# Kernel optimization log

Hardware: AMD Instinct MI355X
Metric: run time of the kernel (lower is better)

## Reference

```python
import jax, jax.numpy as jnp
import numpy as np

NUM_LEVELS = 16
LOG2_T = 19
TABLE_SIZE = 1 << LOG2_T
F_PER_LEVEL = 2
MIN_RES, MAX_RES = 16, 4096
N = 524288

_growth = np.exp((np.log(MAX_RES) - np.log(MIN_RES)) / (NUM_LEVELS - 1))
SCALINGS = np.floor(MIN_RES * _growth ** np.arange(NUM_LEVELS)).astype(np.float32)  # [L]
HASH_OFFSET = (np.arange(NUM_LEVELS) * TABLE_SIZE).astype(np.uint32)  # [L]
# corner selection: True -> use ceil coord, order matches torch hashed_0..hashed_7
CORNER_MASK = np.array([[1,1,1],[1,0,1],[0,0,1],[0,1,1],[1,1,0],[1,0,0],[0,0,0],[0,1,0]], dtype=bool)
PRIMES = np.array([1, 2654435761, 805459861], dtype=np.uint32)


def _hash(coords):
    # coords: uint32 [..., 3]; instant-ngp spatial hash, table size is a power of 2
    c = coords * jnp.asarray(PRIMES)
    h = c[..., 0] ^ c[..., 1] ^ c[..., 2]
    h = h & jnp.uint32(TABLE_SIZE - 1)
    return (h + jnp.asarray(HASH_OFFSET)).astype(jnp.int32)  # [..., L]


def hash_encode(pts, table):
    # pts: [N, 3] in [0,1]; table: [L*T, F]
    scaled = pts[:, None, :] * jnp.asarray(SCALINGS)[:, None]            # [N, L, 3]
    sc = jnp.ceil(scaled).astype(jnp.int32).astype(jnp.uint32)
    sf_f = jnp.floor(scaled)
    sf = sf_f.astype(jnp.int32).astype(jnp.uint32)
    offset = scaled - sf_f                                               # [N, L, 3]
    mask = jnp.asarray(CORNER_MASK)[:, None, None, :]                    # [8,1,1,3]
    coords = jnp.where(mask, sc[None], sf[None])                         # [8, N, L, 3]
    f = table[_hash(coords)]                                             # [8, N, L, F]
    wx = offset[..., 0:1]; wy = offset[..., 1:2]; wz = offset[..., 2:3]
    f_03 = f[0] * wx + f[3] * (1 - wx)
    f_12 = f[1] * wx + f[2] * (1 - wx)
    f_56 = f[5] * wx + f[6] * (1 - wx)
    f_47 = f[4] * wx + f[7] * (1 - wx)
    f0312 = f_03 * wy + f_12 * (1 - wy)
    f4756 = f_47 * wy + f_56 * (1 - wy)
    enc = f0312 * wz + f4756 * (1 - wz)                                  # [N, L, F]
    return enc.reshape(enc.shape[0], NUM_LEVELS * F_PER_LEVEL)


def setup_inputs() -> dict:
    key = jax.random.key(0)
    k1, k2, k3, k4 = jax.random.split(key, 4)
    x = jax.random.uniform(k1, (N, 6), dtype=jnp.float32)
    hash_table = (jax.random.uniform(k2, (TABLE_SIZE * NUM_LEVELS, F_PER_LEVEL), dtype=jnp.float32) * 2 - 1) * 1e-3
    w1 = jax.random.normal(k3, (64, 64), dtype=jnp.float32) * 0.05
    w2 = jax.random.normal(k4, (64, 16), dtype=jnp.float32) * 0.05
    return {"x": x, "hash_table": hash_table, "w1": w1, "w2": w2}


def reference(x, hash_table, w1, w2):
    p0, p1 = x[:, :3], x[:, 3:]                          # segment start / end
    enc = jnp.concatenate([hash_encode(p0, hash_table), hash_encode(p1, hash_table)], axis=-1)  # [N,64]
    h = jax.nn.relu(enc @ w1)                            # FullyFusedMLP: 1 hidden layer, ReLU, no bias
    out = h @ w2                                         # [N, 1+geo_feat_dim]
    density = jnp.exp(out[:, :1] - 1.0)                  # trunc_exp(x - 1)
    return jnp.concatenate([density, out[:, 1:]], axis=-1)
```

## Files before the change

kernel.cpp:

```cpp
#include <hip/hip_runtime.h>
#include <math.h>

#define NLVL 16
#define TSIZE (1u << 19)
#define PRIME_Y 2654435761u
#define PRIME_Z 805459861u
#define QSCALE 126000.0f
#define W1SCALE 254.0f

#if __has_builtin(__builtin_amdgcn_sdot4)
#define HAS_SDOT4 1
#else
#define HAS_SDOT4 0
#endif
#if __has_builtin(__builtin_amdgcn_fdot2)
#define HAS_FDOT2 1
#else
#define HAS_FDOT2 0
#endif

typedef _Float16 half2_t __attribute__((ext_vector_type(2)));

struct ScalingsArg { float s[NLVL]; };

__device__ __forceinline__ unsigned f2bf(float f) {
    unsigned u = __float_as_uint(f);
    return (u + 0x7fffu + ((u >> 16) & 1u)) >> 16;
}
__device__ __forceinline__ float bf2f(unsigned hw) { return __uint_as_float(hw << 16); }

__device__ __forceinline__ int q8(float v) {
    return __float2int_rn(fmaxf(fminf(v * QSCALE, 127.f), -127.f));
}
__device__ __forceinline__ unsigned qw8(float v) {
    return (unsigned)(__float2int_rn(fmaxf(fminf(v * W1SCALE, 127.f), -127.f))) & 0xffu;
}

__device__ __forceinline__ int dot4i8(unsigned a, unsigned b, int c) {
#if HAS_SDOT4
    return __builtin_amdgcn_sdot4((int)a, (int)b, c, false);
#else
    c += (int)(signed char)(a & 0xffu)         * (int)(signed char)(b & 0xffu);
    c += (int)(signed char)((a >> 8) & 0xffu)  * (int)(signed char)((b >> 8) & 0xffu);
    c += (int)(signed char)((a >> 16) & 0xffu) * (int)(signed char)((b >> 16) & 0xffu);
    c += (int)(signed char)(a >> 24)           * (int)(signed char)(b >> 24);
    return c;
#endif
}

__device__ __forceinline__ unsigned pkh2(float a, float b) {
    union { half2_t h; unsigned u; } cv;
    cv.h.x = (_Float16)a; cv.h.y = (_Float16)b;
    return cv.u;
}
__device__ __forceinline__ float dot2h(unsigned a, unsigned b, float c) {
    union { unsigned u; half2_t h; } ca, cb;
    ca.u = a; cb.u = b;
#if HAS_FDOT2
    return __builtin_amdgcn_fdot2(ca.h, cb.h, c, false);
#else
    return c + (float)ca.h.x * (float)cb.h.x + (float)ca.h.y * (float)cb.h.y;
#endif
}

__global__ __launch_bounds__(256) void ngp_conv(
    const float4* __restrict__ t, uint2* __restrict__ o, int n2)
{
    const int i = blockIdx.x * 256 + threadIdx.x;
    if (i < n2) {
        const float4 v = t[i];
        o[i] = make_uint2(f2bf(v.x) | (f2bf(v.y) << 16),
                          f2bf(v.z) | (f2bf(v.w) << 16));
    }
}

template<int BF>
__global__ __launch_bounds__(256) void ngp_encode_lvl(
    const float* __restrict__ x,
    const float2* __restrict__ tf,
    const unsigned* __restrict__ tb,
    unsigned* __restrict__ encq,
    ScalingsArg sca, int npts)
{
    const int pt = blockIdx.x * 256 + threadIdx.x;
    if (pt >= npts) return;
    const int l = blockIdx.y;
    const float s = sca.s[l];
    const unsigned base = (unsigned)l * TSIZE;
    const unsigned m = TSIZE - 1u;

    const float* xp = x + (size_t)pt * 6;
    const float2 v0 = *reinterpret_cast<const float2*>(xp);
    const float2 v1 = *reinterpret_cast<const float2*>(xp + 2);
    const float2 v2 = *reinterpret_cast<const float2*>(xp + 4);
    const float q[2][3] = { { v0.x, v0.y, v1.x }, { v1.y, v2.x, v2.y } };

    int qb[4];
    #pragma unroll
    for (int e = 0; e < 2; ++e) {
        const float sx = q[e][0] * s, sy = q[e][1] * s, sz = q[e][2] * s;
        const float fx = floorf(sx), fy = floorf(sy), fz = floorf(sz);
        const float wx = sx - fx, wy = sy - fy, wz = sz - fz;
        const unsigned ixf = (unsigned)(int)fx, iyf = (unsigned)(int)fy, izf = (unsigned)(int)fz;
        const unsigned ixc = (unsigned)(int)ceilf(sx);
        const unsigned iyc = (unsigned)(int)ceilf(sy);
        const unsigned izc = (unsigned)(int)ceilf(sz);
        const unsigned hyf = iyf * PRIME_Y, hyc = iyc * PRIME_Y;
        const unsigned hzf = izf * PRIME_Z, hzc = izc * PRIME_Z;
        const unsigned h0 = hyc ^ hzc, h1 = hyf ^ hzc, h2 = hyf ^ hzf, h3 = hyc ^ hzf;
        const unsigned dx = ixf ^ ixc;
        const unsigned A[4] = { (ixf ^ h0) & m, (ixf ^ h1) & m,
                                (ixf ^ h2) & m, (ixf ^ h3) & m };

        float2 cf[4], cc[4];

        if (BF) {
            unsigned uf[4], uc[4];
            if (dx == 1u) {
                #pragma unroll
                for (int j = 0; j < 4; ++j) {
                    const uint2 v = *reinterpret_cast<const uint2*>(&tb[base + (A[j] & ~1u)]);
                    const bool hi = (A[j] & 1u) != 0u;
                    uf[j] = hi ? v.y : v.x;
                    uc[j] = hi ? v.x : v.y;
                }
            } else if (dx == 3u) {
                #pragma unroll
                for (int j = 0; j < 4; ++j) {
                    const uint4 v = *reinterpret_cast<const uint4*>(&tb[base + (A[j] & ~3u)]);
                    const unsigned o = A[j] & 3u;
                    uf[j] = (o == 0u) ? v.x : (o == 1u) ? v.y : (o == 2u) ? v.z : v.w;
                    uc[j] = (o == 0u) ? v.w : (o == 1u) ? v.z : (o == 2u) ? v.y : v.x;
                }
            } else {
                #pragma unroll
                for (int j = 0; j < 4; ++j) {
                    uf[j] = tb[base + A[j]];
                    uc[j] = tb[base + ((A[j] ^ dx) & m)];
                }
            }
            #pragma unroll
            for (int j = 0; j < 4; ++j) {
                cf[j] = make_float2(bf2f(uf[j] & 0xffffu), bf2f(uf[j] >> 16));
                cc[j] = make_float2(bf2f(uc[j] & 0xffffu), bf2f(uc[j] >> 16));
            }
        } else {
            if (dx == 1u) {
                #pragma unroll
                for (int j = 0; j < 4; ++j) {
                    const float4 v = *reinterpret_cast<const float4*>(&tf[base + (A[j] & ~1u)]);
                    const bool hi = (A[j] & 1u) != 0u;
                    cf[j] = hi ? make_float2(v.z, v.w) : make_float2(v.x, v.y);
                    cc[j] = hi ? make_float2(v.x, v.y) : make_float2(v.z, v.w);
                }
            } else {
                #pragma unroll
                for (int j = 0; j < 4; ++j) {
                    cf[j] = tf[base + A[j]];
                    cc[j] = tf[base + ((A[j] ^ dx) & m)];
                }
            }
        }

        const float cx = 1.f - wx, cy = 1.f - wy, cz = 1.f - wz;
        const float g03x = cc[0].x * wx + cf[0].x * cx, g03y = cc[0].y * wx + cf[0].y * cx;
        const float g12x = cc[1].x * wx + cf[1].x * cx, g12y = cc[1].y * wx + cf[1].y * cx;
        const float g56x = cc[2].x * wx + cf[2].x * cx, g56y = cc[2].y * wx + cf[2].y * cx;
        const float g47x = cc[3].x * wx + cf[3].x * cx, g47y = cc[3].y * wx + cf[3].y * cx;
        const float t0x = g03x * wy + g12x * cy, t0y = g03y * wy + g12y * cy;
        const float t1x = g47x * wy + g56x * cy, t1y = g47y * wy + g56y * cy;
        qb[e * 2 + 0] = q8(t0x * wz + t1x * cz);
        qb[e * 2 + 1] = q8(t0y * wz + t1y * cz);
    }

    encq[(size_t)l * npts + pt] =
        (qb[0] & 0xff) | ((qb[1] & 0xff) << 8) | ((qb[2] & 0xff) << 16) | ((qb[3] & 0xff) << 24);
}

__global__ __launch_bounds__(256) void ngp_mlp2i(
    const unsigned* __restrict__ encq,
    const float* __restrict__ w1,
    const float* __restrict__ w2,
    float* __restrict__ out, int npts)
{
    __shared__ unsigned lw1i[64 * 16];
    __shared__ unsigned lw2h[16 * 32];
    const int tid = threadIdx.x;

    #pragma unroll
    for (int t = 0; t < 4; ++t) {
        const int idx = tid * 4 + t;
        const int j = idx >> 4, g = idx & 15;
        const unsigned b0 = qw8(w1[(2 * g) * 64 + j]);
        const unsigned b1 = qw8(w1[(2 * g + 1) * 64 + j]);
        const unsigned b2 = qw8(w1[(32 + 2 * g) * 64 + j]);
        const unsigned b3 = qw8(w1[(33 + 2 * g) * 64 + j]);
        lw1i[j * 16 + g] = b0 | (b1 << 8) | (b2 << 16) | (b3 << 24);
    }
    #pragma unroll
    for (int t = 0; t < 2; ++t) {
        const int idx = tid * 2 + t;
        const int c = idx >> 5, jp = idx & 31;
        lw2h[c * 32 + jp] = pkh2(w2[(2 * jp) * 16 + c], w2[(2 * jp + 1) * 16 + c]);
    }
    __syncthreads();

    const int base = (blockIdx.x * 256 + tid) * 2;
    if (base >= npts) return;

    unsigned ev0[16], ev1[16];
    #pragma unroll
    for (int l = 0; l < NLVL; ++l) {
        const uint2 v = *reinterpret_cast<const uint2*>(&encq[(size_t)l * npts + base]);
        ev0[l] = v.x; ev1[l] = v.y;
    }

    const float s1 = 1.0f / (QSCALE * W1SCALE);
    unsigned hp0[32], hp1[32];
    #pragma unroll
    for (int jp = 0; jp < 32; ++jp) {
        const int j0 = 2 * jp, j1 = 2 * jp + 1;
        int a00 = 0, a10 = 0, a01 = 0, a11 = 0;
        #pragma unroll
        for (int g4 = 0; g4 < 4; ++g4) {
            const uint4 w = *reinterpret_cast<const uint4*>(&lw1i[j0 * 16 + g4 * 4]);
            a00 = dot4i8(ev0[g4 * 4 + 0], w.x, a00); a10 = dot4i8(ev1[g4 * 4 + 0], w.x, a10);
            a00 = dot4i8(ev0[g4 * 4 + 1], w.y, a00); a10 = dot4i8(ev1[g4 * 4 + 1], w.y, a10);
            a00 = dot4i8(ev0[g4 * 4 + 2], w.z, a00); a10 = dot4i8(ev1[g4 * 4 + 2], w.z, a10);
            a00 = dot4i8(ev0[g4 * 4 + 3], w.w, a00); a10 = dot4i8(ev1[g4 * 4 + 3], w.w, a10);
        }
        #pragma unroll
        for (int g4 = 0; g4 < 4; ++g4) {
            const uint4 w = *reinterpret_cast<const uint4*>(&lw1i[j1 * 16 + g4 * 4]);
            a01 = dot4i8(ev0[g4 * 4 + 0], w.x, a01); a11 = dot4i8(ev1[g4 * 4 + 0], w.x, a11);
            a01 = dot4i8(ev0[g4 * 4 + 1], w.y, a01); a11 = dot4i8(ev1[g4 * 4 + 1], w.y, a11);
            a01 = dot4i8(ev0[g4 * 4 + 2], w.z, a01); a11 = dot4i8(ev1[g4 * 4 + 2], w.z, a11);
            a01 = dot4i8(ev0[g4 * 4 + 3], w.w, a01); a11 = dot4i8(ev1[g4 * 4 + 3], w.w, a11);
        }
        hp0[jp] = pkh2(fmaxf((float)a00, 0.f) * s1, fmaxf((float)a01, 0.f) * s1);
        hp1[jp] = pkh2(fmaxf((float)a10, 0.f) * s1, fmaxf((float)a11, 0.f) * s1);
    }

    float* op0 = out + (size_t)base * 16;
    const bool p1 = (base + 1 < npts);
    for (int c = 0; c < 16; ++c) {
        float s0 = 0.f, s1v = 0.f;
        #pragma unroll
        for (int jq = 0; jq < 8; ++jq) {
            const uint4 w = *reinterpret_cast<const uint4*>(&lw2h[c * 32 + jq * 4]);
            s0  = dot2h(hp0[jq * 4 + 0], w.x, s0);  s1v = dot2h(hp1[jq * 4 + 0], w.x, s1v);
            s0  = dot2h(hp0[jq * 4 + 1], w.y, s0);  s1v = dot2h(hp1[jq * 4 + 1], w.y, s1v);
            s0  = dot2h(hp0[jq * 4 + 2], w.z, s0);  s1v = dot2h(hp1[jq * 4 + 2], w.z, s1v);
            s0  = dot2h(hp0[jq * 4 + 3], w.w, s0);  s1v = dot2h(hp1[jq * 4 + 3], w.w, s1v);
        }
        if (c == 0) { s0 = expf(s0 - 1.0f); s1v = expf(s1v - 1.0f); }
        op0[c] = s0;
        if (p1) op0[16 + c] = s1v;
    }
}

__global__ __launch_bounds__(256) void ngp_fused(
    const float* __restrict__ x,
    const float2* __restrict__ table,
    const float* __restrict__ w1,
    const float* __restrict__ w2,
    float* __restrict__ out,
    ScalingsArg sca, int npts)
{
    __shared__ float lw1[64 * 64];
    __shared__ float lw2[64 * 16];
    const int tid = threadIdx.x;
    #pragma unroll
    for (int i = 0; i < 16; ++i) lw1[tid + 256 * i] = w1[tid + 256 * i];
    #pragma unroll
    for (int i = 0; i < 4; ++i)  lw2[tid + 256 * i] = w2[tid + 256 * i];
    __syncthreads();

    const int gid = blockIdx.x * 256 + tid;
    if (gid >= npts) return;

    const float* xp = x + (size_t)gid * 6;
    float2 v0 = *reinterpret_cast<const float2*>(xp);
    float2 v1 = *reinterpret_cast<const float2*>(xp + 2);
    float2 v2 = *reinterpret_cast<const float2*>(xp + 4);
    float Pt[6] = { v0.x, v0.y, v1.x, v1.y, v2.x, v2.y };

    float enc[64];
    #pragma unroll
    for (int p = 0; p < 2; ++p) {
        const float qx = Pt[p * 3 + 0], qy = Pt[p * 3 + 1], qz = Pt[p * 3 + 2];
        #pragma unroll
        for (int l = 0; l < NLVL; ++l) {
            const float s = sca.s[l];
            const float sx = qx * s, sy = qy * s, sz = qz * s;
            const float fx = floorf(sx), fy = floorf(sy), fz = floorf(sz);
            const float wx = sx - fx, wy = sy - fy, wz = sz - fz;
            const unsigned ixf = (unsigned)(int)fx, iyf = (unsigned)(int)fy, izf = (unsigned)(int)fz;
            const unsigned ixc = (unsigned)(int)ceilf(sx);
            const unsigned iyc = (unsigned)(int)ceilf(sy);
            const unsigned izc = (unsigned)(int)ceilf(sz);
            const unsigned hyf = iyf * PRIME_Y, hyc = iyc * PRIME_Y;
            const unsigned hzf = izf * PRIME_Z, hzc = izc * PRIME_Z;
            const unsigned mm = TSIZE - 1u;
            const unsigned bs = (unsigned)l * TSIZE;
            const float2 f0 = table[((ixc ^ hyc ^ hzc) & mm) + bs];
            const float2 f1 = table[((ixc ^ hyf ^ hzc) & mm) + bs];
            const float2 f2 = table[((ixf ^ hyf ^ hzc) & mm) + bs];
            const float2 f3 = table[((ixf ^ hyc ^ hzc) & mm) + bs];
            const float2 f4 = table[((ixc ^ hyc ^ hzf) & mm) + bs];
            const float2 f5 = table[((ixc ^ hyf ^ hzf) & mm) + bs];
            const float2 f6 = table[((ixf ^ hyf ^ hzf) & mm) + bs];
            const float2 f7 = table[((ixf ^ hyc ^ hzf) & mm) + bs];
            const float cx = 1.f - wx, cy = 1.f - wy, cz = 1.f - wz;
            const float g03x = f0.x * wx + f3.x * cx, g03y = f0.y * wx + f3.y * cx;
            const float g12x = f1.x * wx + f2.x * cx, g12y = f1.y * wx + f2.y * cx;
            const float g56x = f5.x * wx + f6.x * cx, g56y = f5.y * wx + f6.y * cx;
            const float g47x = f4.x * wx + f7.x * cx, g47y = f4.y * wx + f7.y * cx;
            const float t0x = g03x * wy + g12x * cy, t0y = g03y * wy + g12y * cy;
            const float t1x = g47x * wy + g56x * cy, t1y = g47y * wy + g56y * cy;
            enc[p * 32 + l * 2 + 0] = t0x * wz + t1x * cz;
            enc[p * 32 + l * 2 + 1] = t0y * wz + t1y * cz;
        }
    }

    float o[16];
    #pragma unroll
    for (int i = 0; i < 16; ++i) o[i] = 0.f;
    for (int jb = 0; jb < 64; jb += 8) {
        float acc[8];
        #pragma unroll
        for (int jj = 0; jj < 8; ++jj) acc[jj] = 0.f;
        #pragma unroll
        for (int k = 0; k < 64; ++k) {
            const float e = enc[k];
            const float4* wrow = reinterpret_cast<const float4*>(&lw1[k * 64 + jb]);
            const float4 wa = wrow[0], wb = wrow[1];
            acc[0] += e * wa.x; acc[1] += e * wa.y; acc[2] += e * wa.z; acc[3] += e * wa.w;
            acc[4] += e * wb.x; acc[5] += e * wb.y; acc[6] += e * wb.z; acc[7] += e * wb.w;
        }
        #pragma unroll
        for (int jj = 0; jj < 8; ++jj) {
            const float hv = fmaxf(acc[jj], 0.f);
            const float4* w2row = reinterpret_cast<const float4*>(&lw2[(jb + jj) * 16]);
            const float4 wa = w2row[0], wb = w2row[1], wc = w2row[2], wd = w2row[3];
            o[0]  += hv * wa.x; o[1]  += hv * wa.y; o[2]  += hv * wa.z; o[3]  += hv * wa.w;
            o[4]  += hv * wb.x; o[5]  += hv * wb.y; o[6]  += hv * wb.z; o[7]  += hv * wb.w;
            o[8]  += hv * wc.x; o[9]  += hv * wc.y; o[10] += hv * wc.z; o[11] += hv * wc.w;
            o[12] += hv * wd.x; o[13] += hv * wd.y; o[14] += hv * wd.z; o[15] += hv * wd.w;
        }
    }
    o[0] = expf(o[0] - 1.0f);
    float4* op = reinterpret_cast<float4*>(out + (size_t)gid * 16);
    op[0] = make_float4(o[0],  o[1],  o[2],  o[3]);
    op[1] = make_float4(o[4],  o[5],  o[6],  o[7]);
    op[2] = make_float4(o[8],  o[9],  o[10], o[11]);
    op[3] = make_float4(o[12], o[13], o[14], o[15]);
}

extern "C" void kernel_launch(void* const* d_in, const int* in_sizes, int n_in,
                              void* d_out, int out_size, void* d_ws, size_t ws_size,
                              hipStream_t stream) {
    const float*  x     = (const float*)d_in[0];
    const float2* table = (const float2*)d_in[1];
    const float*  w1    = (const float*)d_in[2];
    const float*  w2    = (const float*)d_in[3];
    float* out = (float*)d_out;
    const int npts = in_sizes[0] / 6;

    ScalingsArg sca;
    const double growth = exp((log(4096.0) - log(16.0)) / 15.0);
    for (int i = 0; i < NLVL; ++i)
        sca.s[i] = (float)floor(16.0 * pow(growth, (double)i));

    const size_t tbl_bytes = (size_t)NLVL * TSIZE * 4u;
    const size_t enc_bytes = (size_t)NLVL * (size_t)npts * 4u;
    const int bpl = (npts + 255) / 256;
    const dim3 gEnc(bpl, NLVL);
    const int mlp_blocks = ((npts + 1) / 2 + 255) / 256;

    if (ws_size >= tbl_bytes + enc_bytes) {
        unsigned* tb  = (unsigned*)d_ws;
        unsigned* enc = (unsigned*)((char*)d_ws + tbl_bytes);
        const int n2 = (NLVL * TSIZE) / 2;
        ngp_conv<<<(n2 + 255) / 256, 256, 0, stream>>>((const float4*)table, (uint2*)tb, n2);
        ngp_encode_lvl<1><<<gEnc, 256, 0, stream>>>(x, nullptr, tb, enc, sca, npts);
        ngp_mlp2i<<<mlp_blocks, 256, 0, stream>>>(enc, w1, w2, out, npts);
    } else if (ws_size >= enc_bytes) {
        unsigned* enc = (unsigned*)d_ws;
        ngp_encode_lvl<0><<<gEnc, 256, 0, stream>>>(x, table, nullptr, enc, sca, npts);
        ngp_mlp2i<<<mlp_blocks, 256, 0, stream>>>(enc, w1, w2, out, npts);
    } else {
        ngp_fused<<<(npts + 255) / 256, 256, 0, stream>>>(x, table, w1, w2, out, sca, npts);
    }
}
```

Measured before the change: 390.5 us.

## Use dense corner-quad grids for coarse levels and block-aligned loads for fine levels

For the four coarsest levels, a new kernel precomputes dense per-cell quads of the four xy-corner bf16 entries, so each encode point fetches two 16-byte records instead of eight scattered hashed entries. Only the remaining twelve levels are converted to bf16. Fine levels now always load one aligned uint4 block that serves both x-corners when they fall in the same block, with a fallback load otherwise. The cost is an extra precompute kernel, a larger workspace, and a level-dependent branch inside the encode kernel.

```diff
diff --git a/kernel.cpp b/kernel.cpp
--- a/kernel.cpp
+++ b/kernel.cpp
@@ -22,12 +22,14 @@
 typedef _Float16 half2_t __attribute__((ext_vector_type(2)));
 
 struct ScalingsArg { float s[NLVL]; };
+struct QuadArg { int off[4]; int res[4]; };
 
 __device__ __forceinline__ unsigned f2bf(float f) {
     unsigned u = __float_as_uint(f);
     return (u + 0x7fffu + ((u >> 16) & 1u)) >> 16;
 }
 __device__ __forceinline__ float bf2f(unsigned hw) { return __uint_as_float(hw << 16); }
+__device__ __forceinline__ unsigned pkbf2(float2 v) { return f2bf(v.x) | (f2bf(v.y) << 16); }
 
 __device__ __forceinline__ int q8(float v) {
     return __float2int_rn(fmaxf(fminf(v * QSCALE, 127.f), -127.f));
@@ -63,15 +65,138 @@
 #endif
 }
 
-__global__ __launch_bounds__(256) void ngp_conv(
-    const float4* __restrict__ t, uint2* __restrict__ o, int n2)
+__device__ __forceinline__ unsigned pick4(uint4 q, int sel) {
+    const unsigned a = (sel & 1) ? q.y : q.x;
+    const unsigned b = (sel & 1) ? q.w : q.z;
+    return (sel & 2) ? b : a;
+}
+
+__global__ __launch_bounds__(256) void ngp_conv12(
+    const float4* __restrict__ src, uint2* __restrict__ o, int n2)
 {
     const int i = blockIdx.x * 256 + threadIdx.x;
     if (i < n2) {
-        const float4 v = t[i];
+        const float4 v = src[i];
         o[i] = make_uint2(f2bf(v.x) | (f2bf(v.y) << 16),
                           f2bf(v.z) | (f2bf(v.w) << 16));
     }
+}
+
+__global__ __launch_bounds__(256) void ngp_quad(
+    const float2* __restrict__ tf, uint4* __restrict__ quads, QuadArg qa)
+{
+    const int l = blockIdx.y;
+    const int res = qa.res[l];
+    const int n = (res + 1) * res * res;
+    const int idx = blockIdx.x * 256 + threadIdx.x;
+    if (idx >= n) return;
+    const int xq = idx % res;
+    const int t1 = idx / res;
+    const int yq = t1 % res;
+    const int zq = t1 / res;
+    const unsigned m = TSIZE - 1u;
+    const unsigned base = (unsigned)l * TSIZE;
+    const unsigned hy0 = (unsigned)yq * PRIME_Y, hy1 = (unsigned)(yq + 1) * PRIME_Y;
+    const unsigned hz  = (unsigned)zq * PRIME_Z;
+    const unsigned x0 = (unsigned)xq, x1 = (unsigned)(xq + 1);
+    const float2 e00 = tf[((x0 ^ hy0 ^ hz) & m) + base];
+    const float2 e10 = tf[((x1 ^ hy0 ^ hz) & m) + base];
+    const float2 e01 = tf[((x0 ^ hy1 ^ hz) & m) + base];
+    const float2 e11 = tf[((x1 ^ hy1 ^ hz) & m) + base];
+    quads[qa.off[l] + idx] = make_uint4(pkbf2(e00), pkbf2(e10), pkbf2(e01), pkbf2(e11));
+}
+
+__global__ __launch_bounds__(256) void ngp_encode2(
+    const float* __restrict__ x,
+    const unsigned* __restrict__ tbHi,
+    const uint4* __restrict__ quads,
+    unsigned* __restrict__ encq,
+    ScalingsArg sca, QuadArg qa, int npts)
+{
+    const int pt = blockIdx.x * 256 + threadIdx.x;
+    if (pt >= npts) return;
+    const int l = blockIdx.y;
+    const float s = sca.s[l];
+    const unsigned m = TSIZE - 1u;
+
+    const float* xp = x + (size_t)pt * 6;
+    const float2 v0 = *reinterpret_cast<const float2*>(xp);
+    const float2 v1 = *reinterpret_cast<const float2*>(xp + 2);
+    const float2 v2 = *reinterpret_cast<const float2*>(xp + 4);
+    const float q[2][3] = { { v0.x, v0.y, v1.x }, { v1.y, v2.x, v2.y } };
+
+    int qb[4];
+    #pragma unroll
+    for (int e = 0; e < 2; ++e) {
+        const float sx = q[e][0] * s, sy = q[e][1] * s, sz = q[e][2] * s;
+        const float fx = floorf(sx), fy = floorf(sy), fz = floorf(sz);
+        const float wx = sx - fx, wy = sy - fy, wz = sz - fz;
+        const unsigned ixf = (unsigned)(int)fx, iyf = (unsigned)(int)fy, izf = (unsigned)(int)fz;
+        const unsigned ixc = (unsigned)(int)ceilf(sx);
+        const unsigned iyc = (unsigned)(int)ceilf(sy);
+        const unsigned izc = (unsigned)(int)ceilf(sz);
+
+        float2 cc[4], cf[4];
+
+        if (l < 4) {
+            const int res = qa.res[l];
+            const int dxs = (int)(ixc - ixf);
+            const int dys = (int)(iyc - iyf);
+            const uint4* Q = quads + qa.off[l];
+            const int rowf = (int)iyf * res + (int)ixf;
+            const uint4 qzc = Q[(int)izc * (res * res) + rowf];
+            const uint4 qzf = Q[(int)izf * (res * res) + rowf];
+            const int selcc = dys * 2 + dxs;
+            const int selfc = dys * 2;
+            const int selcf = dxs;
+            const unsigned u0 = pick4(qzc, selcc);
+            const unsigned u1 = pick4(qzc, selcf);
+            const unsigned u2 = qzc.x;
+            const unsigned u3 = pick4(qzc, selfc);
+            const unsigned u4 = pick4(qzf, selcc);
+            const unsigned u5 = pick4(qzf, selcf);
+            const unsigned u6 = qzf.x;
+            const unsigned u7 = pick4(qzf, selfc);
+            cc[0] = make_float2(bf2f(u0 & 0xffffu), bf2f(u0 >> 16));
+            cf[0] = make_float2(bf2f(u3 & 0xffffu), bf2f(u3 >> 16));
+            cc[1] = make_float2(bf2f(u1 & 0xffffu), bf2f(u1 >> 16));
+            cf[1] = make_float2(bf2f(u2 & 0xffffu), bf2f(u2 >> 16));
+            cc[2] = make_float2(bf2f(u5 & 0xffffu), bf2f(u5 >> 16));
+            cf[2] = make_float2(bf2f(u6 & 0xffffu), bf2f(u6 >> 16));
+            cc[3] = make_float2(bf2f(u4 & 0xffffu), bf2f(u4 >> 16));
+            cf[3] = make_float2(bf2f(u7 & 0xffffu), bf2f(u7 >> 16));
+        } else {
+            const unsigned base = (unsigned)(l - 4) * TSIZE;
+            const unsigned hyf = iyf * PRIME_Y, hyc = iyc * PRIME_Y;
+            const unsigned hzf = izf * PRIME_Z, hzc = izc * PRIME_Z;
+            const unsigned H[4] = { hyc ^ hzc, hyf ^ hzc, hyf ^ hzf, hyc ^ hzf };
+            const unsigned dx = ixf ^ ixc;
+            #pragma unroll
+            for (int j = 0; j < 4; ++j) {
+                const unsigned A  = (ixf ^ H[j]) & m;
+                const unsigned Ax = A ^ dx;
+                const uint4 blk = *reinterpret_cast<const uint4*>(&tbHi[base + (A & ~3u)]);
+                const unsigned uf = pick4(blk, (int)(A & 3u));
+                unsigned uc = pick4(blk, (int)(Ax & 3u));
+                if (dx > 3u) uc = tbHi[base + Ax];
+                cf[j] = make_float2(bf2f(uf & 0xffffu), bf2f(uf >> 16));
+                cc[j] = make_float2(bf2f(uc & 0xffffu), bf2f(uc >> 16));
+            }
+        }
+
+        const float cx = 1.f - wx, cy = 1.f - wy, cz = 1.f - wz;
+        const float g03x = cc[0].x * wx + cf[0].x * cx, g03y = cc[0].y * wx + cf[0].y * cx;
+        const float g12x = cc[1].x * wx + cf[1].x * cx, g12y = cc[1].y * wx + cf[1].y * cx;
+        const float g56x = cc[2].x * wx + cf[2].x * cx, g56y = cc[2].y * wx + cf[2].y * cx;
+        const float g47x = cc[3].x * wx + cf[3].x * cx, g47y = cc[3].y * wx + cf[3].y * cx;
+        const float t0x = g03x * wy + g12x * cy, t0y = g03y * wy + g12y * cy;
+        const float t1x = g47x * wy + g56x * cy, t1y = g47y * wy + g56y * cy;
+        qb[e * 2 + 0] = q8(t0x * wz + t1x * cz);
+        qb[e * 2 + 1] = q8(t0y * wz + t1y * cz);
+    }
+
+    encq[(size_t)l * npts + pt] =
+        (qb[0] & 0xff) | ((qb[1] & 0xff) << 8) | ((qb[2] & 0xff) << 16) | ((qb[3] & 0xff) << 24);
 }
 
 template<int BF>
@@ -111,57 +236,22 @@
         const unsigned dx = ixf ^ ixc;
         const unsigned A[4] = { (ixf ^ h0) & m, (ixf ^ h1) & m,
                                 (ixf ^ h2) & m, (ixf ^ h3) & m };
-
         float2 cf[4], cc[4];
-
-        if (BF) {
-            unsigned uf[4], uc[4];
-            if (dx == 1u) {
-                #pragma unroll
-                for (int j = 0; j < 4; ++j) {
-                    const uint2 v = *reinterpret_cast<const uint2*>(&tb[base + (A[j] & ~1u)]);
-                    const bool hi = (A[j] & 1u) != 0u;
-                    uf[j] = hi ? v.y : v.x;
-                    uc[j] = hi ? v.x : v.y;
-                }
-            } else if (dx == 3u) {
-                #pragma unroll
-                for (int j = 0; j < 4; ++j) {
-                    const uint4 v = *reinterpret_cast<const uint4*>(&tb[base + (A[j] & ~3u)]);
-                    const unsigned o = A[j] & 3u;
-                    uf[j] = (o == 0u) ? v.x : (o == 1u) ? v.y : (o == 2u) ? v.z : v.w;
-                    uc[j] = (o == 0u) ? v.w : (o == 1u) ? v.z : (o == 2u) ? v.y : v.x;
-                }
-            } else {
-                #pragma unroll
-                for (int j = 0; j < 4; ++j) {
-                    uf[j] = tb[base + A[j]];
-                    uc[j] = tb[base + ((A[j] ^ dx) & m)];
-                }
-            }
+        if (dx == 1u) {
             #pragma unroll
             for (int j = 0; j < 4; ++j) {
-                cf[j] = make_float2(bf2f(uf[j] & 0xffffu), bf2f(uf[j] >> 16));
-                cc[j] = make_float2(bf2f(uc[j] & 0xffffu), bf2f(uc[j] >> 16));
+                const float4 v = *reinterpret_cast<const float4*>(&tf[base + (A[j] & ~1u)]);
+                const bool hi = (A[j] & 1u) != 0u;
+                cf[j] = hi ? make_float2(v.z, v.w) : make_float2(v.x, v.y);
+                cc[j] = hi ? make_float2(v.x, v.y) : make_float2(v.z, v.w);
             }
         } else {
-            if (dx == 1u) {
-                #pragma unroll
-                for (int j = 0; j < 4; ++j) {
-                    const float4 v = *reinterpret_cast<const float4*>(&tf[base + (A[j] & ~1u)]);
-                    const bool hi = (A[j] & 1u) != 0u;
-                    cf[j] = hi ? make_float2(v.z, v.w) : make_float2(v.x, v.y);
-                    cc[j] = hi ? make_float2(v.x, v.y) : make_float2(v.z, v.w);
-                }
-            } else {
-                #pragma unroll
-                for (int j = 0; j < 4; ++j) {
-                    cf[j] = tf[base + A[j]];
-                    cc[j] = tf[base + ((A[j] ^ dx) & m)];
-                }
+            #pragma unroll
+            for (int j = 0; j < 4; ++j) {
+                cf[j] = tf[base + A[j]];
+                cc[j] = tf[base + ((A[j] ^ dx) & m)];
             }
         }
-
         const float cx = 1.f - wx, cy = 1.f - wy, cz = 1.f - wz;
         const float g03x = cc[0].x * wx + cf[0].x * cx, g03y = cc[0].y * wx + cf[0].y * cx;
         const float g12x = cc[1].x * wx + cf[1].x * cx, g12y = cc[1].y * wx + cf[1].y * cx;
@@ -172,7 +262,6 @@
         qb[e * 2 + 0] = q8(t0x * wz + t1x * cz);
         qb[e * 2 + 1] = q8(t0y * wz + t1y * cz);
     }
-
     encq[(size_t)l * npts + pt] =
         (qb[0] & 0xff) | ((qb[1] & 0xff) << 8) | ((qb[2] & 0xff) << 16) | ((qb[3] & 0xff) << 24);
 }
@@ -372,18 +461,33 @@
     for (int i = 0; i < NLVL; ++i)
         sca.s[i] = (float)floor(16.0 * pow(growth, (double)i));
 
-    const size_t tbl_bytes = (size_t)NLVL * TSIZE * 4u;
-    const size_t enc_bytes = (size_t)NLVL * (size_t)npts * 4u;
+    QuadArg qa;
+    int qtot = 0, qmax = 0;
+    for (int l = 0; l < 4; ++l) {
+        const int r = (int)sca.s[l];
+        qa.res[l] = r;
+        qa.off[l] = qtot;
+        const int n = (r + 1) * r * r;
+        qtot += n;
+        if (n > qmax) qmax = n;
+    }
+
+    const size_t tbhi_bytes = (size_t)12 * TSIZE * 4u;
+    const size_t enc_bytes  = (size_t)NLVL * (size_t)npts * 4u;
+    const size_t quad_bytes = (size_t)qtot * 16u;
     const int bpl = (npts + 255) / 256;
     const dim3 gEnc(bpl, NLVL);
     const int mlp_blocks = ((npts + 1) / 2 + 255) / 256;
 
-    if (ws_size >= tbl_bytes + enc_bytes) {
-        unsigned* tb  = (unsigned*)d_ws;
-        unsigned* enc = (unsigned*)((char*)d_ws + tbl_bytes);
-        const int n2 = (NLVL * TSIZE) / 2;
-        ngp_conv<<<(n2 + 255) / 256, 256, 0, stream>>>((const float4*)table, (uint2*)tb, n2);
-        ngp_encode_lvl<1><<<gEnc, 256, 0, stream>>>(x, nullptr, tb, enc, sca, npts);
+    if (ws_size >= tbhi_bytes + enc_bytes + quad_bytes) {
+        unsigned* tbHi = (unsigned*)d_ws;
+        unsigned* enc  = (unsigned*)((char*)d_ws + tbhi_bytes);
+        uint4*    quads = (uint4*)((char*)d_ws + tbhi_bytes + enc_bytes);
+        const int n2 = (12 * TSIZE) / 2;
+        ngp_conv12<<<(n2 + 255) / 256, 256, 0, stream>>>(
+            (const float4*)(table + (size_t)4 * TSIZE), (uint2*)tbHi, n2);
+        ngp_quad<<<dim3((qmax + 255) / 256, 4), 256, 0, stream>>>(table, quads, qa);
+        ngp_encode2<<<gEnc, 256, 0, stream>>>(x, tbHi, quads, enc, sca, qa, npts);
         ngp_mlp2i<<<mlp_blocks, 256, 0, stream>>>(enc, w1, w2, out, npts);
     } else if (ws_size >= enc_bytes) {
         unsigned* enc = (unsigned*)d_ws;
```

Result: faster. 363.6 us (-6.9%).
